# Performance work log

Hardware: AMD Instinct MI355X
Metric: run time of the kernel (lower is better)

## Reference

```python
import jax, jax.numpy as jnp
import numpy as np

N = 20000        # num nodes
E = 320000       # num edges (avg degree 16)
INPUT_DIM = 256
D = 512          # d_model
FF = 2048        # dim_feedforward
OUT = 128        # output_linear out features
HDIM = 8         # LiteMLA per-head dim
KS = 5           # LiteMLA scale kernel size (scales=(5,))


def _layernorm(x, g, b, eps=1e-5):
    m = x.mean(-1, keepdims=True)
    v = ((x - m) ** 2).mean(-1, keepdims=True)
    return (x - m) * jax.lax.rsqrt(v + eps) * g + b


def _pos_encoding():
    # sin/cos table, d_model even branch of PositionalEncoding
    pos = np.arange(N, dtype=np.float32)[:, None]
    div = np.exp(np.arange(0, D, 2, dtype=np.float32) * (-np.log(10000.0) / D))
    pe = np.zeros((N, D), np.float32)
    pe[:, 0::2] = np.sin(pos * div)
    pe[:, 1::2] = np.cos(pos * div)
    return jnp.asarray(pe)


def _lite_mla(h, W_qkv, conv_w, W_proj, b_proj):
    # ReLU linear attention with one extra conv scale (kernel 5), per EfficientViT LiteMLA
    n, d = h.shape
    qkv = h @ W_qkv                               # [N, 3D]
    xc = qkv.T[None]                              # [1, 3D, N]
    ms = jax.lax.conv_general_dilated(
        xc, conv_w, window_strides=(1,), padding='SAME',
        feature_group_count=3 * D)                # depthwise conv over node axis
    ms = ms[0].T                                  # [N, 3D]
    full = jnp.concatenate([qkv, ms], axis=1)     # [N, 6D]
    heads = full.shape[1] // (3 * HDIM)           # 2 * D / HDIM
    t = full.reshape(n, heads, 3, HDIM)
    q = jax.nn.relu(t[:, :, 0])
    k = jax.nn.relu(t[:, :, 1])
    v = t[:, :, 2]
    v1 = jnp.concatenate([v, jnp.ones_like(v[..., :1])], axis=-1)  # append denom row
    kv = jnp.einsum('nhd,nhe->hde', k, v1)        # [h, HDIM, HDIM+1]
    o = jnp.einsum('nhd,hde->nhe', q, kv)         # [N, h, HDIM+1]
    o = o[..., :HDIM] / (o[..., HDIM:] + 1e-15)
    o = o.reshape(n, heads * HDIM)                # [N, 2D]
    return o @ W_proj + b_proj


def _fwd(x, edge_attr, pe, W_in, b_in, W_qkv, conv_w, W_proj, b_proj,
         g1, beta1, W1, bf1, W2, bf2, g2, beta2, W_out, b_out,
         edge_index, num_nodes):
    n = num_nodes
    h = x @ W_in + b_in
    h = h + pe[:n]                                # positional encoding (dropout=eval)
    # add self loops with weight 1
    loop = jnp.arange(n)
    row = jnp.concatenate([edge_index[0], loop])
    col = jnp.concatenate([edge_index[1], loop])
    w = jnp.concatenate([edge_attr, jnp.ones((n,), edge_attr.dtype)])
    # symmetric normalization: D^-1/2 W D^-1/2
    deg = jax.ops.segment_sum(w, row, num_segments=n)
    dis = jnp.where(deg > 0, jax.lax.rsqrt(jnp.maximum(deg, 1e-12)), 0.0)
    nw = dis[row] * w * dis[col]
    # attention + FFN (post-norm residuals as written)
    src2 = _lite_mla(h, W_qkv, conv_w, W_proj, b_proj)
    src = h + _layernorm(src2, g1, beta1)
    ff = jax.nn.relu(src @ W1 + bf1) @ W2 + bf2
    src = src + _layernorm(ff, g2, beta2)
    # sparse adjacency matmul: out[i] = sum_{e: row=i} nw_e * src[col_e]
    agg = jax.ops.segment_sum(nw[:, None] * src[col], row, num_segments=n)
    return jax.nn.relu(agg) @ W_out + b_out      # [N, OUT]


def setup_inputs() -> dict:
    key = jax.random.key(0)
    ks = jax.random.split(key, 10)
    s = lambda i, *sh: jax.random.normal(ks[i], sh, jnp.float32) * 0.02
    f32 = jnp.float32
    return {
        'x': jax.random.normal(ks[0], (N, INPUT_DIM), f32),
        'edge_index': jax.random.randint(ks[1], (2, E), 0, N),
        'edge_attr': jax.random.uniform(ks[2], (E,), f32),
        'num_nodes': N,
        'pe': _pos_encoding(),
        'W_in': s(3, INPUT_DIM, D), 'b_in': jnp.zeros((D,), f32),
        'W_qkv': s(4, D, 3 * D),
        'conv_w': s(5, 3 * D, 1, KS),
        'W_proj': s(6, 2 * D, D), 'b_proj': jnp.zeros((D,), f32),
        'g1': jnp.ones((D,), f32), 'beta1': jnp.zeros((D,), f32),
        'W1': s(7, D, FF), 'bf1': jnp.zeros((FF,), f32),
        'W2': s(8, FF, D), 'bf2': jnp.zeros((D,), f32),
        'g2': jnp.ones((D,), f32), 'beta2': jnp.zeros((D,), f32),
        'W_out': s(9, D, OUT), 'b_out': jnp.zeros((OUT,), f32),
    }


def reference(x, edge_index, edge_attr, num_nodes, pe, W_in, b_in, W_qkv, conv_w,
              W_proj, b_proj, g1, beta1, W1, bf1, W2, bf2, g2, beta2, W_out, b_out):
    return _fwd(x, edge_attr, pe, W_in, b_in, W_qkv, conv_w, W_proj, b_proj,
                g1, beta1, W1, bf1, W2, bf2, g2, beta2, W_out, b_out,
                edge_index, num_nodes)
```

## Files before the change

kernel.cpp:

```cpp
#include <hip/hip_runtime.h>

#define N_NODES 20000
#define N_EDGES 320000
#define DIN     256
#define DMODEL  512
#define TD      1536
#define FFD     2048
#define DOUT    128

typedef _Float16 f16;
typedef f16 f16x8 __attribute__((ext_vector_type(8)));
typedef f16 f16x4 __attribute__((ext_vector_type(4)));
typedef f16 f16x2 __attribute__((ext_vector_type(2)));
typedef float f32x4 __attribute__((ext_vector_type(4)));

__device__ __forceinline__ void cstore(float* p, float v) { *p = v; }
__device__ __forceinline__ void cstore(f16* p, float v)   { *p = (f16)v; }

#if defined(__has_builtin)
#if __has_builtin(__builtin_amdgcn_global_load_lds)
#define USE_GLOAD_LDS 1
#endif
#endif

template<typename TC, int HAS_BIAS, int HAS_ADD, int DO_RELU>
__global__ __launch_bounds__(256)
void gemm_mfma(const f16* __restrict__ A, const f16* __restrict__ Bt,
               const float* __restrict__ bias, const float* __restrict__ addmat,
               TC* __restrict__ C, f16* __restrict__ Cbf,
               int M, int N, int K)
{
    __shared__ f16 As[128 * 32];
    __shared__ f16 Bs[128 * 32];
    const int tid  = threadIdx.x;
    const int lane = tid & 63;
    const int wid  = tid >> 6;
    const int wm = wid >> 1, wn = wid & 1;
    const int m0 = blockIdx.y * 128, n0 = blockIdx.x * 128;

    f32x4 acc[4][4];
    #pragma unroll
    for (int i = 0; i < 4; ++i)
        #pragma unroll
        for (int j = 0; j < 4; ++j)
            acc[i][j] = (f32x4)0.0f;

    const int r  = lane & 15;
    const int kg = lane >> 4;
    const int px = (kg ^ ((r >> 1) & 3)) << 3;

    for (int k0 = 0; k0 < K; k0 += 32) {
#ifdef USE_GLOAD_LDS
        #pragma unroll
        for (int j = 0; j < 2; ++j) {
            const int seg  = wid * 2 + j;
            const int row  = seg * 16 + (lane >> 2);
            const int kc   = (lane & 3) ^ ((row >> 1) & 3);
            const f16* asrc = A  + (size_t)(m0 + row) * K + k0 + kc * 8;
            const f16* bsrc = Bt + (size_t)(n0 + row) * K + k0 + kc * 8;
            __builtin_amdgcn_global_load_lds(
                (const __attribute__((address_space(1))) void*)asrc,
                (__attribute__((address_space(3))) void*)&As[seg * 512], 16, 0, 0);
            __builtin_amdgcn_global_load_lds(
                (const __attribute__((address_space(1))) void*)bsrc,
                (__attribute__((address_space(3))) void*)&Bs[seg * 512], 16, 0, 0);
        }
#else
        #pragma unroll
        for (int it = 0; it < 2; ++it) {
            const int c   = tid + it * 256;
            const int row = c >> 2, kc = c & 3;
            const int widx = row * 32 + ((kc ^ ((row >> 1) & 3)) << 3);
            f16x8 va = {0, 0, 0, 0, 0, 0, 0, 0};
            const int ga = m0 + row;
            if (ga < M) va = *(const f16x8*)(A + (size_t)ga * K + k0 + kc * 8);
            *(f16x8*)(&As[widx]) = va;
            const f16x8 vb = *(const f16x8*)(Bt + (size_t)(n0 + row) * K + k0 + kc * 8);
            *(f16x8*)(&Bs[widx]) = vb;
        }
#endif
        __syncthreads();
        f16x8 af[4], bfr[4];
        #pragma unroll
        for (int m = 0; m < 4; ++m)
            af[m] = *(const f16x8*)(&As[(wm * 64 + m * 16 + r) * 32 + px]);
        #pragma unroll
        for (int n = 0; n < 4; ++n)
            bfr[n] = *(const f16x8*)(&Bs[(wn * 64 + n * 16 + r) * 32 + px]);
        #pragma unroll
        for (int m = 0; m < 4; ++m)
            #pragma unroll
            for (int n = 0; n < 4; ++n)
                acc[m][n] = __builtin_amdgcn_mfma_f32_16x16x32_f16(
                    af[m], bfr[n], acc[m][n], 0, 0, 0);
        __syncthreads();
    }

    const int rq = lane >> 4;
    #pragma unroll
    for (int m = 0; m < 4; ++m) {
        #pragma unroll
        for (int rr = 0; rr < 4; ++rr) {
            const int row = m0 + wm * 64 + m * 16 + rq * 4 + rr;
            if (row >= M) continue;
            #pragma unroll
            for (int n = 0; n < 4; ++n) {
                const int col = n0 + wn * 64 + n * 16 + (lane & 15);
                float v = acc[m][n][rr];
                if (HAS_BIAS) v += bias[col];
                if (HAS_ADD)  v += addmat[(size_t)row * N + col];
                if (DO_RELU)  v = fmaxf(v, 0.f);
                cstore(&C[(size_t)row * N + col], v);
                if (Cbf) Cbf[(size_t)row * N + col] = (f16)v;
            }
        }
    }
}

__global__ void wt_kernel(const float* __restrict__ W, f16* __restrict__ Wt, int K, int N)
{
    __shared__ float t[32][33];
    const int k0 = blockIdx.x * 32, n0 = blockIdx.y * 32;
    const int tx = threadIdx.x & 31, ty = threadIdx.x >> 5;
    #pragma unroll
    for (int i = ty; i < 32; i += 8) {
        const int k = k0 + i;
        if (k < K && n0 + tx < N) t[i][tx] = W[(size_t)k * N + n0 + tx];
    }
    __syncthreads();
    #pragma unroll
    for (int i = ty; i < 32; i += 8) {
        const int n = n0 + i;
        if (n < N && k0 + tx < K) Wt[(size_t)n * K + k0 + tx] = (f16)t[tx][i];
    }
}

__global__ void f2h_kernel(const float* __restrict__ in, f16* __restrict__ out, int n)
{
    const int i = (blockIdx.x * 256 + threadIdx.x) * 4;
    if (i < n) {
        const float4 v = *(const float4*)(in + i);
        out[i + 0] = (f16)v.x; out[i + 1] = (f16)v.y;
        out[i + 2] = (f16)v.z; out[i + 3] = (f16)v.w;
    }
}

#define KV_CHUNK 32
#define KV_BLOCKS (N_NODES / KV_CHUNK)
__global__ __launch_bounds__(256, 2)
void kv_fused_kernel(const f16* __restrict__ qkv, const float* __restrict__ cw,
                     f16* __restrict__ q_all, float* __restrict__ kvg,
                     float* __restrict__ kv_part)
{
    __shared__ f16 rows[5][TD];
    const int tid = threadIdx.x;
    const int n0 = blockIdx.x * KV_CHUNK;
    const int h = tid >> 1, d0 = (tid & 1) * 4;

    float wk[4][5], wv[8][5], wq[8][5];
    if (h >= 64) {
        const int cb = (h - 64) * 24;
        #pragma unroll
        for (int dd = 0; dd < 4; ++dd)
            #pragma unroll
            for (int t = 0; t < 5; ++t)
                wk[dd][t] = cw[(cb + 8 + d0 + dd) * 5 + t];
        #pragma unroll
        for (int e = 0; e < 8; ++e)
            #pragma unroll
            for (int t = 0; t < 5; ++t)
                wv[e][t] = cw[(cb + 16 + e) * 5 + t];
    }
    if (tid >= 64 && tid < 128) {
        const int cb = (tid - 64) * 24;
        #pragma unroll
        for (int d = 0; d < 8; ++d)
            #pragma unroll
            for (int t = 0; t < 5; ++t)
                wq[d][t] = cw[(cb + d) * 5 + t];
    }

    for (int r = n0 - 2; r <= n0 + 2; ++r) {
        const int slot = ((r % 5) + 5) % 5;
        if (tid < 192) {
            f16x8 v = {0, 0, 0, 0, 0, 0, 0, 0};
            if (r >= 0 && r < N_NODES)
                v = *(const f16x8*)(qkv + (size_t)r * TD + tid * 8);
            *(f16x8*)(&rows[slot][tid * 8]) = v;
        }
    }
    __syncthreads();

    float acc[36] = {};

    for (int i = 0; i < KV_CHUNK; ++i) {
        const int n = n0 + i;

        f16x8 pre = {0, 0, 0, 0, 0, 0, 0, 0};
        const bool doPre = (i < KV_CHUNK - 1) && (tid < 192);
        if (doPre && (n + 3) < N_NODES)
            pre = *(const f16x8*)(qkv + (size_t)(n + 3) * TD + tid * 8);

        const f16* wr[5] = { rows[(((n - 2) % 5) + 5) % 5],
                             rows[(((n - 1) % 5) + 5) % 5],
                             rows[n % 5],
                             rows[(n + 1) % 5],
                             rows[(n + 2) % 5] };

        float kv4[4], vv[8];
        if (h < 64) {
            const int cb = h * 24;
            const f16x4 kd = *(const f16x4*)(wr[2] + cb + 8 + d0);
            const f16x8 vd = *(const f16x8*)(wr[2] + cb + 16);
            #pragma unroll
            for (int dd = 0; dd < 4; ++dd) kv4[dd] = fmaxf((float)kd[dd], 0.f);
            #pragma unroll
            for (int e = 0; e < 8; ++e) vv[e] = (float)vd[e];
        } else {
            const int cb = (h - 64) * 24;
            f16x4 ka[5]; f16x8 va[5];
            #pragma unroll
            for (int t = 0; t < 5; ++t) {
                ka[t] = *(const f16x4*)(wr[t] + cb + 8 + d0);
                va[t] = *(const f16x8*)(wr[t] + cb + 16);
            }
            #pragma unroll
            for (int dd = 0; dd < 4; ++dd) {
                float s = 0.f;
                #pragma unroll
                for (int t = 0; t < 5; ++t) s = fmaf(wk[dd][t], (float)ka[t][dd], s);
                kv4[dd] = fmaxf(s, 0.f);
            }
            #pragma unroll
            for (int e = 0; e < 8; ++e) {
                float s = 0.f;
                #pragma unroll
                for (int t = 0; t < 5; ++t) s = fmaf(wv[e][t], (float)va[t][e], s);
                vv[e] = s;
            }
        }
        #pragma unroll
        for (int dd = 0; dd < 4; ++dd) {
            #pragma unroll
            for (int e = 0; e < 8; ++e)
                acc[dd * 9 + e] = fmaf(kv4[dd], vv[e], acc[dd * 9 + e]);
            acc[dd * 9 + 8] += kv4[dd];
        }

        if (tid < 128) {
            f16x8 qv;
            if (tid < 64) {
                qv = *(const f16x8*)(wr[2] + tid * 24);
                #pragma unroll
                for (int d = 0; d < 8; ++d)
                    qv[d] = qv[d] > (f16)0 ? qv[d] : (f16)0;
            } else {
                const int cb = (tid - 64) * 24;
                f16x8 qa[5];
                #pragma unroll
                for (int t = 0; t < 5; ++t) qa[t] = *(const f16x8*)(wr[t] + cb);
                #pragma unroll
                for (int d = 0; d < 8; ++d) {
                    float s = 0.f;
                    #pragma unroll
                    for (int t = 0; t < 5; ++t) s = fmaf(wq[d][t], (float)qa[t][d], s);
                    qv[d] = (f16)fmaxf(s, 0.f);
                }
            }
            *(f16x8*)(q_all + (size_t)n * 1024 + tid * 8) = qv;
        }

        __syncthreads();
        if (doPre)
            *(f16x8*)(&rows[(n + 3) % 5][tid * 8]) = pre;
        __syncthreads();
    }

    if (kv_part) {
        float* dst = kv_part + (size_t)blockIdx.x * 9216 + tid * 36;
        #pragma unroll
        for (int i = 0; i < 36; ++i) dst[i] = acc[i];
    } else {
        #pragma unroll
        for (int dd = 0; dd < 4; ++dd)
            #pragma unroll
            for (int e = 0; e < 9; ++e)
                atomicAdd(&kvg[h * 72 + (d0 + dd) * 9 + e], acc[dd * 9 + e]);
    }
}

__global__ void kv_reduce_kernel(const float* __restrict__ kv_part,
                                 float* __restrict__ kvg)
{
    const int j = blockIdx.x * 256 + threadIdx.x;
    float s = 0.f;
    for (int b = 0; b < KV_BLOCKS; ++b)
        s += kv_part[(size_t)b * 9216 + j];
    kvg[j] = s;
}

__global__ __launch_bounds__(256)
void attn_o_kernel(const f16* __restrict__ q_all, const float* __restrict__ kvg,
                   f16* __restrict__ o)
{
    __shared__ float kvt[72][128];
    const int tid = threadIdx.x;
    for (int i = tid; i < 9216; i += 256) {
        const int hh = i & 127, j = i >> 7;
        kvt[j][hh] = kvg[hh * 72 + j];
    }
    __syncthreads();
    const int h = tid & 127, sub = tid >> 7;
    for (int nb = blockIdx.x; nb < N_NODES / 2; nb += gridDim.x) {
        const int n = nb * 2 + sub;
        const f16x8 qv8 = *(const f16x8*)(q_all + (size_t)n * 1024 + h * 8);
        float q[8];
        #pragma unroll
        for (int d = 0; d < 8; ++d) q[d] = (float)qv8[d];
        float num[8], den = 0.f;
        #pragma unroll
        for (int e = 0; e < 8; ++e) {
            float s = 0.f;
            #pragma unroll
            for (int d = 0; d < 8; ++d) s = fmaf(q[d], kvt[d * 9 + e][h], s);
            num[e] = s;
        }
        #pragma unroll
        for (int d = 0; d < 8; ++d) den = fmaf(q[d], kvt[d * 9 + 8][h], den);
        const float rinv = 1.f / (den + 1e-15f);
        f16x8 ov;
        #pragma unroll
        for (int e = 0; e < 8; ++e) ov[e] = (f16)(num[e] * rinv);
        *(f16x8*)(o + (size_t)n * 1024 + h * 8) = ov;
    }
}

__global__ void ln_res_kernel(const f16* __restrict__ y, const f16* __restrict__ resid,
                              const float* __restrict__ g, const float* __restrict__ b,
                              f16* __restrict__ out_h)
{
    const int row = blockIdx.x;
    const int tid = threadIdx.x;
    const f16* yr = y + (size_t)row * DMODEL;
    const float v0 = (float)yr[tid], v1 = (float)yr[tid + 256];
    __shared__ float red[4], red2[4];
    float s = v0 + v1;
    #pragma unroll
    for (int o = 32; o > 0; o >>= 1) s += __shfl_down(s, o);
    if ((tid & 63) == 0) red[tid >> 6] = s;
    __syncthreads();
    const float mean = (red[0] + red[1] + red[2] + red[3]) * (1.0f / DMODEL);
    const float d0 = v0 - mean, d1 = v1 - mean;
    float q = d0 * d0 + d1 * d1;
    #pragma unroll
    for (int o = 32; o > 0; o >>= 1) q += __shfl_down(q, o);
    if ((tid & 63) == 0) red2[tid >> 6] = q;
    __syncthreads();
    const float var = (red2[0] + red2[1] + red2[2] + red2[3]) * (1.0f / DMODEL);
    const float inv = rsqrtf(var + 1e-5f);
    const f16* rr = resid + (size_t)row * DMODEL;
    const float o0 = (float)rr[tid]       + d0 * inv * g[tid]       + b[tid];
    const float o1 = (float)rr[tid + 256] + d1 * inv * g[tid + 256] + b[tid + 256];
    f16* oh = out_h + (size_t)row * DMODEL;
    oh[tid] = (f16)o0;
    oh[tid + 256] = (f16)o1;
}

__global__ void deg_init_kernel(float* __restrict__ deg)
{
    const int i = blockIdx.x * 256 + threadIdx.x;
    if (i < N_NODES) deg[i] = 1.0f;
}

__global__ void deg_acc_kernel(const int* __restrict__ eirow, const float* __restrict__ ea,
                               float* __restrict__ deg)
{
    const int e = blockIdx.x * 256 + threadIdx.x;
    if (e < N_EDGES) atomicAdd(&deg[eirow[e]], ea[e]);
}

__global__ void dis_kernel(const float* __restrict__ deg, float* __restrict__ dis)
{
    const int i = blockIdx.x * 256 + threadIdx.x;
    if (i < N_NODES) dis[i] = rsqrtf(deg[i]);
}

__global__ void count_kernel(const int* __restrict__ eirow, int* __restrict__ cnt)
{
    const int e = blockIdx.x * 256 + threadIdx.x;
    if (e < N_EDGES) atomicAdd(&cnt[eirow[e]], 1);
}

__global__ void scan_kernel(const int* __restrict__ cnt, int* __restrict__ rowstart,
                            int* __restrict__ cursor)
{
    __shared__ int ls[1024];
    const int tid = threadIdx.x;
    const int base = tid * 20;
    int local[20];
    int s = 0;
    #pragma unroll
    for (int i = 0; i < 20; ++i) {
        const int idx = base + i;
        const int v = (idx < N_NODES) ? cnt[idx] : 0;
        local[i] = s;
        s += v;
    }
    ls[tid] = s;
    __syncthreads();
    for (int off = 1; off < 1024; off <<= 1) {
        const int v = (tid >= off) ? ls[tid - off] : 0;
        __syncthreads();
        ls[tid] += v;
        __syncthreads();
    }
    const int excl = (tid == 0) ? 0 : ls[tid - 1];
    #pragma unroll
    for (int i = 0; i < 20; ++i) {
        const int idx = base + i;
        if (idx < N_NODES) {
            const int st = excl + local[i];
            rowstart[idx] = st;
            cursor[idx] = st;
        }
    }
    if (tid == 1023) rowstart[N_NODES] = ls[1023];
}

__global__ void scatter_kernel(const int* __restrict__ eirow, int* __restrict__ cursor,
                               int* __restrict__ sorted)
{
    const int e = blockIdx.x * 256 + threadIdx.x;
    if (e < N_EDGES) {
        const int r = eirow[e];
        const int p = atomicAdd(&cursor[r], 1);
        sorted[p] = e;
    }
}

__global__ __launch_bounds__(256)
void agg_kernel(const f16* __restrict__ srcf_h, const int* __restrict__ eicol,
                const float* __restrict__ ea, const float* __restrict__ dis,
                const int* __restrict__ rowstart, const int* __restrict__ sorted,
                f16* __restrict__ agg)
{
    __shared__ int   cbuf[256];
    __shared__ float wbuf[256];
    __shared__ float part[4][512];
    const int i = blockIdx.x;
    const int tid = threadIdx.x;
    const int lane = tid & 63, wv = tid >> 6;
    const float di = dis[i];
    const int s = rowstart[i];
    const int deg = rowstart[i + 1] - s;

    float acc[8] = {};
    for (int base = 0; base < deg; base += 256) {
        const int m = min(256, deg - base);
        if (tid < m) {
            const int e = sorted[s + base + tid];
            const int c = eicol[e];
            cbuf[tid] = c;
            wbuf[tid] = di * ea[e] * dis[c];
        }
        __syncthreads();
        #pragma unroll 2
        for (int p = wv; p < m; p += 4) {
            const int c = cbuf[p];
            const float w = wbuf[p];
            const f16x8 v = *(const f16x8*)(srcf_h + (size_t)c * DMODEL + lane * 8);
            #pragma unroll
            for (int j = 0; j < 8; ++j) acc[j] = fmaf(w, (float)v[j], acc[j]);
        }
        __syncthreads();
    }
    #pragma unroll
    for (int j = 0; j < 8; ++j) part[wv][lane * 8 + j] = acc[j];
    __syncthreads();
    const float wself = di * di;
    const f16x2 vs = *(const f16x2*)(srcf_h + (size_t)i * DMODEL + tid * 2);
    float a0 = wself * (float)vs[0], a1 = wself * (float)vs[1];
    #pragma unroll
    for (int w = 0; w < 4; ++w) {
        a0 += part[w][tid * 2];
        a1 += part[w][tid * 2 + 1];
    }
    f16x2 o;
    o[0] = (f16)fmaxf(a0, 0.f);
    o[1] = (f16)fmaxf(a1, 0.f);
    *(f16x2*)(agg + (size_t)i * DMODEL + tid * 2) = o;
}

static constexpr size_t OFF_HH    = 0;
static constexpr size_t OFF_FF    = 20480000ull;
static constexpr size_t OFF_QKV   = 40960000ull;
static constexpr size_t OFF_SRC2  = 40960000ull;
static constexpr size_t OFF_FFH   = 61440000ull;
static constexpr size_t OFF_AGG   = 61440000ull;
static constexpr size_t OFF_XH    = 102400000ull;
static constexpr size_t OFF_ATTN  = 102400000ull;
static constexpr size_t WT_IN     = 143360000ull;
static constexpr size_t WT_QKV    = 143622144ull;
static constexpr size_t WT_PROJ   = 145195008ull;
static constexpr size_t WT_W1     = 146243584ull;
static constexpr size_t WT_W2     = 148340736ull;
static constexpr size_t WT_OUT    = 150437888ull;
static constexpr size_t OFF_KV    = 150568960ull;
static constexpr size_t OFF_DEG   = 150605824ull;
static constexpr size_t OFF_DIS   = 150685824ull;
static constexpr size_t OFF_RS    = 150765824ull;
static constexpr size_t OFF_CUR   = 150845888ull;
static constexpr size_t OFF_CNT   = 150925888ull;
static constexpr size_t OFF_SORT  = 151005888ull;
static constexpr size_t OFF_KVP   = 152285888ull;
static constexpr size_t WS_NEED_KVP = 175325888ull;

extern "C" void kernel_launch(void* const* d_in, const int* in_sizes, int n_in,
                              void* d_out, int out_size, void* d_ws, size_t ws_size,
                              hipStream_t stream)
{
    const float* x      = (const float*)d_in[0];
    const int*   ei     = (const int*)d_in[1];
    const float* ea     = (const float*)d_in[2];
    const float* pe     = (const float*)d_in[4];
    const float* W_in   = (const float*)d_in[5];
    const float* b_in   = (const float*)d_in[6];
    const float* W_qkv  = (const float*)d_in[7];
    const float* conv_w = (const float*)d_in[8];
    const float* W_proj = (const float*)d_in[9];
    const float* b_proj = (const float*)d_in[10];
    const float* g1     = (const float*)d_in[11];
    const float* beta1  = (const float*)d_in[12];
    const float* W1     = (const float*)d_in[13];
    const float* bf1    = (const float*)d_in[14];
    const float* W2     = (const float*)d_in[15];
    const float* bf2    = (const float*)d_in[16];
    const float* g2     = (const float*)d_in[17];
    const float* beta2  = (const float*)d_in[18];
    const float* W_out  = (const float*)d_in[19];
    const float* b_out  = (const float*)d_in[20];

    char* ws = (char*)d_ws;
    f16*   h_h    = (f16*)(ws + OFF_HH);
    f16*   ff     = (f16*)(ws + OFF_FF);
    f16*   qkv    = (f16*)(ws + OFF_QKV);
    f16*   src2   = (f16*)(ws + OFF_SRC2);
    f16*   ffh    = (f16*)(ws + OFF_FFH);
    f16*   agg    = (f16*)(ws + OFF_AGG);
    f16*   x_h    = (f16*)(ws + OFF_XH);
    f16*   q_all  = (f16*)(ws + OFF_ATTN);
    f16*   wt_in   = (f16*)(ws + WT_IN);
    f16*   wt_qkv  = (f16*)(ws + WT_QKV);
    f16*   wt_proj = (f16*)(ws + WT_PROJ);
    f16*   wt_w1   = (f16*)(ws + WT_W1);
    f16*   wt_w2   = (f16*)(ws + WT_W2);
    f16*   wt_out  = (f16*)(ws + WT_OUT);
    float* kvg    = (float*)(ws + OFF_KV);
    float* deg    = (float*)(ws + OFF_DEG);
    float* dis    = (float*)(ws + OFF_DIS);
    int*   rs     = (int*)(ws + OFF_RS);
    int*   cur    = (int*)(ws + OFF_CUR);
    int*   cnt    = (int*)(ws + OFF_CNT);
    int*   sorted = (int*)(ws + OFF_SORT);
    float* outp   = (float*)d_out;

    const bool twoStage = (ws_size >= WS_NEED_KVP);
    float* kv_part = twoStage ? (float*)(ws + OFF_KVP) : nullptr;

    const int* eirow = ei;
    const int* eicol = ei + N_EDGES;

    if (!twoStage)
        hipMemsetAsync(kvg, 0, 9216 * sizeof(float), stream);
    hipMemsetAsync(cnt, 0, N_NODES * sizeof(int), stream);

    wt_kernel<<<dim3(DIN / 32,   DMODEL / 32), 256, 0, stream>>>(W_in,   wt_in,   DIN,    DMODEL);
    wt_kernel<<<dim3(DMODEL / 32, TD / 32),    256, 0, stream>>>(W_qkv,  wt_qkv,  DMODEL, TD);
    wt_kernel<<<dim3(1024 / 32,  DMODEL / 32), 256, 0, stream>>>(W_proj, wt_proj, 1024,   DMODEL);
    wt_kernel<<<dim3(DMODEL / 32, FFD / 32),   256, 0, stream>>>(W1,     wt_w1,   DMODEL, FFD);
    wt_kernel<<<dim3(FFD / 32,   DMODEL / 32), 256, 0, stream>>>(W2,     wt_w2,   FFD,    DMODEL);
    wt_kernel<<<dim3(DMODEL / 32, DOUT / 32),  256, 0, stream>>>(W_out,  wt_out,  DMODEL, DOUT);
    f2h_kernel<<<(N_NODES * DIN) / 1024, 256, 0, stream>>>(x, x_h, N_NODES * DIN);

    const int GY = (N_NODES + 127) / 128;

    gemm_mfma<f16, 1, 1, 0><<<dim3(DMODEL / 128, GY), 256, 0, stream>>>(
        x_h, wt_in, b_in, pe, h_h, nullptr, N_NODES, DMODEL, DIN);
    gemm_mfma<f16, 0, 0, 0><<<dim3(TD / 128, GY), 256, 0, stream>>>(
        h_h, wt_qkv, nullptr, nullptr, qkv, nullptr, N_NODES, TD, DMODEL);
    kv_fused_kernel<<<KV_BLOCKS, 256, 0, stream>>>(qkv, conv_w, q_all, kvg, kv_part);
    if (twoStage)
        kv_reduce_kernel<<<36, 256, 0, stream>>>(kv_part, kvg);
    attn_o_kernel<<<2500, 256, 0, stream>>>(q_all, kvg, q_all);
    gemm_mfma<f16, 1, 0, 0><<<dim3(DMODEL / 128, GY), 256, 0, stream>>>(
        q_all, wt_proj, b_proj, nullptr, src2, nullptr, N_NODES, DMODEL, 1024);
    ln_res_kernel<<<N_NODES, 256, 0, stream>>>(src2, h_h, g1, beta1, src2);
    gemm_mfma<f16, 1, 0, 1><<<dim3(FFD / 128, GY), 256, 0, stream>>>(
        src2, wt_w1, bf1, nullptr, ffh, nullptr, N_NODES, FFD, DMODEL);
    gemm_mfma<f16, 1, 0, 0><<<dim3(DMODEL / 128, GY), 256, 0, stream>>>(
        ffh, wt_w2, bf2, nullptr, ff, nullptr, N_NODES, DMODEL, FFD);
    ln_res_kernel<<<N_NODES, 256, 0, stream>>>(ff, src2, g2, beta2, ff);
    deg_init_kernel<<<(N_NODES + 255) / 256, 256, 0, stream>>>(deg);
    deg_acc_kernel<<<(N_EDGES + 255) / 256, 256, 0, stream>>>(eirow, ea, deg);
    dis_kernel<<<(N_NODES + 255) / 256, 256, 0, stream>>>(deg, dis);
    count_kernel<<<(N_EDGES + 255) / 256, 256, 0, stream>>>(eirow, cnt);
    scan_kernel<<<1, 1024, 0, stream>>>(cnt, rs, cur);
    scatter_kernel<<<(N_EDGES + 255) / 256, 256, 0, stream>>>(eirow, cur, sorted);
    agg_kernel<<<N_NODES, 256, 0, stream>>>(ff, eicol, ea, dis, rs, sorted, agg);
    gemm_mfma<float, 1, 0, 0><<<dim3(DOUT / 128, GY), 256, 0, stream>>>(
        agg, wt_out, b_out, nullptr, outp, nullptr, N_NODES, DOUT, DMODEL);
}
```

Before: 704.0 us.

## Double-buffer LDS tiles in MFMA GEMM with async global-to-LDS prefetch

Adds a second LDS buffer for the A and B tiles in the MFMA GEMM. The next K-tile is prefetched with global_load_lds while the current one is consumed, and a partial vmcnt wait plus explicit barriers keep the two in order. The goal is to hide global memory latency behind MFMA work. It doubles LDS use per block, which may lower occupancy, and it depends on the hand-written waitcnt being correct.

```diff
diff --git a/kernel.cpp b/kernel.cpp
--- a/kernel.cpp
+++ b/kernel.cpp
@@ -30,8 +30,8 @@
                TC* __restrict__ C, f16* __restrict__ Cbf,
                int M, int N, int K)
 {
-    __shared__ f16 As[128 * 32];
-    __shared__ f16 Bs[128 * 32];
+    __shared__ f16 As[2][128 * 32];
+    __shared__ f16 Bs[2][128 * 32];
     const int tid  = threadIdx.x;
     const int lane = tid & 63;
     const int wid  = tid >> 6;
@@ -49,23 +49,62 @@
     const int kg = lane >> 4;
     const int px = (kg ^ ((r >> 1) & 3)) << 3;
 
+#ifdef USE_GLOAD_LDS
+    const int seg0 = wid * 2, seg1 = wid * 2 + 1;
+    const int row0 = seg0 * 16 + (lane >> 2);
+    const int row1 = seg1 * 16 + (lane >> 2);
+    const int kc0  = (lane & 3) ^ ((row0 >> 1) & 3);
+    const int kc1  = (lane & 3) ^ ((row1 >> 1) & 3);
+    const f16* a0 = A  + (size_t)(m0 + row0) * K + kc0 * 8;
+    const f16* a1 = A  + (size_t)(m0 + row1) * K + kc1 * 8;
+    const f16* b0 = Bt + (size_t)(n0 + row0) * K + kc0 * 8;
+    const f16* b1 = Bt + (size_t)(n0 + row1) * K + kc1 * 8;
+
+    auto stage = [&](int buf, int k0) {
+        __builtin_amdgcn_global_load_lds(
+            (const __attribute__((address_space(1))) void*)(a0 + k0),
+            (__attribute__((address_space(3))) void*)&As[buf][seg0 * 512], 16, 0, 0);
+        __builtin_amdgcn_global_load_lds(
+            (const __attribute__((address_space(1))) void*)(a1 + k0),
+            (__attribute__((address_space(3))) void*)&As[buf][seg1 * 512], 16, 0, 0);
+        __builtin_amdgcn_global_load_lds(
+            (const __attribute__((address_space(1))) void*)(b0 + k0),
+            (__attribute__((address_space(3))) void*)&Bs[buf][seg0 * 512], 16, 0, 0);
+        __builtin_amdgcn_global_load_lds(
+            (const __attribute__((address_space(1))) void*)(b1 + k0),
+            (__attribute__((address_space(3))) void*)&Bs[buf][seg1 * 512], 16, 0, 0);
+    };
+
+    const int NT = K >> 5;
+    stage(0, 0);
+    for (int kt = 0; kt < NT; ++kt) {
+        const int cur = kt & 1;
+        if (kt + 1 < NT) {
+            stage(cur ^ 1, (kt + 1) << 5);
+            asm volatile("s_waitcnt vmcnt(4)" ::: "memory");
+        } else {
+            asm volatile("s_waitcnt vmcnt(0)" ::: "memory");
+        }
+        __builtin_amdgcn_s_barrier();
+        __builtin_amdgcn_sched_barrier(0);
+        f16x8 af[4], bfr[4];
+        #pragma unroll
+        for (int m = 0; m < 4; ++m)
+            af[m] = *(const f16x8*)(&As[cur][(wm * 64 + m * 16 + r) * 32 + px]);
+        #pragma unroll
+        for (int n = 0; n < 4; ++n)
+            bfr[n] = *(const f16x8*)(&Bs[cur][(wn * 64 + n * 16 + r) * 32 + px]);
+        #pragma unroll
+        for (int m = 0; m < 4; ++m)
+            #pragma unroll
+            for (int n = 0; n < 4; ++n)
+                acc[m][n] = __builtin_amdgcn_mfma_f32_16x16x32_f16(
+                    af[m], bfr[n], acc[m][n], 0, 0, 0);
+        __builtin_amdgcn_sched_barrier(0);
+        __builtin_amdgcn_s_barrier();
+    }
+#else
     for (int k0 = 0; k0 < K; k0 += 32) {
-#ifdef USE_GLOAD_LDS
-        #pragma unroll
-        for (int j = 0; j < 2; ++j) {
-            const int seg  = wid * 2 + j;
-            const int row  = seg * 16 + (lane >> 2);
-            const int kc   = (lane & 3) ^ ((row >> 1) & 3);
-            const f16* asrc = A  + (size_t)(m0 + row) * K + k0 + kc * 8;
-            const f16* bsrc = Bt + (size_t)(n0 + row) * K + k0 + kc * 8;
-            __builtin_amdgcn_global_load_lds(
-                (const __attribute__((address_space(1))) void*)asrc,
-                (__attribute__((address_space(3))) void*)&As[seg * 512], 16, 0, 0);
-            __builtin_amdgcn_global_load_lds(
-                (const __attribute__((address_space(1))) void*)bsrc,
-                (__attribute__((address_space(3))) void*)&Bs[seg * 512], 16, 0, 0);
-        }
-#else
         #pragma unroll
         for (int it = 0; it < 2; ++it) {
             const int c   = tid + it * 256;
@@ -74,19 +113,18 @@
             f16x8 va = {0, 0, 0, 0, 0, 0, 0, 0};
             const int ga = m0 + row;
             if (ga < M) va = *(const f16x8*)(A + (size_t)ga * K + k0 + kc * 8);
-            *(f16x8*)(&As[widx]) = va;
+            *(f16x8*)(&As[0][widx]) = va;
             const f16x8 vb = *(const f16x8*)(Bt + (size_t)(n0 + row) * K + k0 + kc * 8);
-            *(f16x8*)(&Bs[widx]) = vb;
-        }
-#endif
+            *(f16x8*)(&Bs[0][widx]) = vb;
+        }
         __syncthreads();
         f16x8 af[4], bfr[4];
         #pragma unroll
         for (int m = 0; m < 4; ++m)
-            af[m] = *(const f16x8*)(&As[(wm * 64 + m * 16 + r) * 32 + px]);
+            af[m] = *(const f16x8*)(&As[0][(wm * 64 + m * 16 + r) * 32 + px]);
         #pragma unroll
         for (int n = 0; n < 4; ++n)
-            bfr[n] = *(const f16x8*)(&Bs[(wn * 64 + n * 16 + r) * 32 + px]);
+            bfr[n] = *(const f16x8*)(&Bs[0][(wn * 64 + n * 16 + r) * 32 + px]);
         #pragma unroll
         for (int m = 0; m < 4; ++m)
             #pragma unroll
@@ -95,6 +133,7 @@
                     af[m], bfr[n], acc[m][n], 0, 0, 0);
         __syncthreads();
     }
+#endif
 
     const int rq = lane >> 4;
     #pragma unroll
```

New measurement: 684.0 us. 1.03x faster.
